# Kernel tuning notes

Hardware: AMD Instinct MI355X
Metric: run time of the kernel (lower is better)

## Reference

```python
import jax, jax.numpy as jnp
import numpy as np

F = 256

def setup_inputs() -> dict:
    key = jax.random.key(0)
    ks = jax.random.split(key, 6)
    s = 1.0 / np.sqrt(F)
    x = jax.random.normal(ks[0], (16, 1024, F), dtype=jnp.float32)
    W_alpha = jax.random.uniform(ks[1], (F, F), minval=-s, maxval=s, dtype=jnp.float32)
    W_beta = jax.random.uniform(ks[2], (F, F), minval=-s, maxval=s, dtype=jnp.float32)
    W_unary = jax.random.uniform(ks[3], (F, F), minval=-s, maxval=s, dtype=jnp.float32)
    b_unary = jax.random.uniform(ks[4], (F,), minval=-s, maxval=s, dtype=jnp.float32)
    W_r = jax.random.uniform(ks[5], (F, F), minval=-s, maxval=s, dtype=jnp.float32)
    return {"x": x, "W_alpha": W_alpha, "W_beta": W_beta, "W_unary": W_unary, "b_unary": b_unary, "W_r": W_r}

def reference(x, W_alpha, W_beta, W_unary, b_unary, W_r):
    # x: [B, N, F]; torch Linear computes x @ W^T (+ b)
    B, N, _ = x.shape
    alpha = jnp.einsum('bnf,gf->bng', x, W_alpha)
    beta = jnp.einsum('bnf,gf->bng', x, W_beta)
    unary = jnp.einsum('bnf,gf->bng', x, W_unary) + b_unary
    # scores: alpha_i . beta_j, diagonal excluded (i == j skipped in loop)
    scores = jnp.einsum('bif,bjf->bij', alpha, beta)
    scores = scores * (1.0 - jnp.eye(N, dtype=x.dtype))
    att = jnp.einsum('bij,bjf->bif', scores, unary) / N
    out = jnp.einsum('bif,gf->big', att, W_r) + x
    return out
```

## Files before the change

kernel.cpp:

```cpp
#include <hip/hip_runtime.h>


typedef __bf16 bf16;
typedef float floatx4 __attribute__((ext_vector_type(4)));
typedef bf16 bf16x8 __attribute__((ext_vector_type(8)));
typedef bf16 bf16x4 __attribute__((ext_vector_type(4)));

constexpr int FD = 256;
constexpr int NB = 16;
constexpr int NN = 1024;
constexpr int RR = NB * NN;

__global__ __launch_bounds__(256)
void prep(const float* __restrict__ Wa, const float* __restrict__ Wb,
          const float* __restrict__ Wu, const float* __restrict__ bu, const float* __restrict__ Wr,
          bf16* __restrict__ Wab, bf16* __restrict__ Wbb, bf16* __restrict__ Wcb,
          float* __restrict__ bc)
{
    const int blk = blockIdx.x, tid = threadIdx.x;
    if (blk < 16) {
        int w = blk >> 3, wb = blk & 7;
        const float* src = (w == 0) ? Wa : Wb;
        bf16* dst = (w == 0) ? Wab : Wbb;
        for (int it = 0; it < 8; it++) {
            int i = wb * 8192 + it * 1024 + tid * 4;
            float4 v = *(const float4*)&src[i];
            bf16x4 o = { (bf16)v.x, (bf16)v.y, (bf16)v.z, (bf16)v.w };
            *(bf16x4*)&dst[i] = o;
        }
    } else if (blk < 80) {
        int j0 = (blk - 16) * 4;
        float acc[4] = {};
        for (int g = 0; g < FD; g++) {
            float wu = Wu[g * FD + tid];
            #pragma unroll
            for (int jr = 0; jr < 4; jr++)
                acc[jr] += Wr[(j0 + jr) * FD + g] * wu;
        }
        #pragma unroll
        for (int jr = 0; jr < 4; jr++)
            Wcb[(j0 + jr) * FD + tid] = (bf16)acc[jr];
    } else {
        float s = 0.0f;
        for (int g = 0; g < FD; g++) s += Wr[tid * FD + g] * bu[g];
        bc[tid] = s;
    }
}

__global__ __launch_bounds__(256)
void proj3(const float* __restrict__ x,
           const bf16* __restrict__ W0, const bf16* __restrict__ W1, const bf16* __restrict__ W2,
           bf16* __restrict__ alpha, bf16* __restrict__ U2,
           bf16* __restrict__ betaT, bf16* __restrict__ U2T,
           const float* __restrict__ bc, float* __restrict__ dpart)
{
    constexpr int BM = 128, BN = 64, BK = 32, LDK = 40;
    __shared__ bf16 As[BM][LDK];
    __shared__ bf16 Bs[3][BN][LDK];
    __shared__ bf16 Tr[64][136];
    const int tid = threadIdx.x;
    const int wave = tid >> 6, lane = tid & 63;
    const int q = lane >> 4, l16 = lane & 15;
    const int bm = blockIdx.y * BM, bn = blockIdx.x * BN;
    const bf16* Wp[3] = { W0, W1, W2 };

    floatx4 acc[3][2][4] = {};

    for (int k0 = 0; k0 < FD; k0 += BK) {
        #pragma unroll
        for (int it = 0; it < 2; it++) {
            int c = tid + it * 256;
            int row = c >> 2, k8 = (c & 3) * 8;
            const float* src = &x[(size_t)(bm + row) * FD + k0 + k8];
            float4 v0 = *(const float4*)src;
            float4 v1 = *(const float4*)(src + 4);
            bf16x8 o = { (bf16)v0.x, (bf16)v0.y, (bf16)v0.z, (bf16)v0.w,
                         (bf16)v1.x, (bf16)v1.y, (bf16)v1.z, (bf16)v1.w };
            *(bf16x8*)&As[row][k8] = o;
        }
        #pragma unroll
        for (int w = 0; w < 3; w++) {
            int row = tid >> 2, k8 = (tid & 3) * 8;
            *(int4*)&Bs[w][row][k8] = *(const int4*)&Wp[w][(size_t)(bn + row) * FD + k0 + k8];
        }
        __syncthreads();
        bf16x8 af[2];
        #pragma unroll
        for (int mi = 0; mi < 2; mi++)
            af[mi] = *(const bf16x8*)&As[wave * 32 + mi * 16 + l16][q * 8];
        #pragma unroll
        for (int w = 0; w < 3; w++) {
            bf16x8 bq[4];
            #pragma unroll
            for (int nj = 0; nj < 4; nj++)
                bq[nj] = *(const bf16x8*)&Bs[w][nj * 16 + l16][q * 8];
            #pragma unroll
            for (int mi = 0; mi < 2; mi++)
                #pragma unroll
                for (int nj = 0; nj < 4; nj++)
                    acc[w][mi][nj] = __builtin_amdgcn_mfma_f32_16x16x32_bf16(af[mi], bq[nj], acc[w][mi][nj], 0, 0, 0);
        }
        __syncthreads();
    }

    const int b = bm >> 10, n0 = bm & (NN - 1);

    #pragma unroll
    for (int mi = 0; mi < 2; mi++)
        #pragma unroll
        for (int i = 0; i < 4; i++) {
            int m = bm + wave * 32 + mi * 16 + q * 4 + i;
            #pragma unroll
            for (int nj = 0; nj < 4; nj++) {
                int n = bn + nj * 16 + l16;
                alpha[(size_t)m * FD + n] = (bf16)acc[0][mi][nj][i];
                U2[(size_t)m * FD + n]    = (bf16)(acc[2][mi][nj][i] + bc[n]);
            }
        }

    #pragma unroll
    for (int mi = 0; mi < 2; mi++)
        #pragma unroll
        for (int i = 0; i < 4; i++) {
            float p = 0.0f;
            #pragma unroll
            for (int nj = 0; nj < 4; nj++)
                p += acc[0][mi][nj][i] * acc[1][mi][nj][i];
            #pragma unroll
            for (int off = 1; off < 16; off <<= 1) p += __shfl_xor(p, off);
            if (l16 == 0) {
                int m = bm + wave * 32 + mi * 16 + q * 4 + i;
                dpart[(size_t)blockIdx.x * RR + m] = p;
            }
        }

    #pragma unroll
    for (int w = 1; w < 3; w++) {
        __syncthreads();
        #pragma unroll
        for (int mi = 0; mi < 2; mi++)
            #pragma unroll
            for (int i = 0; i < 4; i++)
                #pragma unroll
                for (int nj = 0; nj < 4; nj++) {
                    float v = acc[w][mi][nj][i];
                    if (w == 2) v += bc[bn + nj * 16 + l16];
                    Tr[nj * 16 + l16][wave * 32 + mi * 16 + q * 4 + i] = (bf16)v;
                }
        __syncthreads();
        bf16* dst = ((w == 1) ? betaT : U2T) + (size_t)b * FD * NN;
        int row = tid >> 2;
        #pragma unroll
        for (int it = 0; it < 4; it++) {
            int chunk = (tid & 3) * 4 + it;
            bf16x8 v = *(const bf16x8*)&Tr[row][chunk * 8];
            *(bf16x8*)&dst[(size_t)(bn + row) * NN + n0 + chunk * 8] = v;
        }
    }
}

__global__ __launch_bounds__(256)
void m2_mfma(const bf16* __restrict__ U2T, const bf16* __restrict__ betaT, bf16* __restrict__ M2t)
{
    constexpr int LDK = 40;
    __shared__ bf16 As[64][LDK];
    __shared__ bf16 Bs[64][LDK];
    const int tid = threadIdx.x;
    const int wave = tid >> 6, lane = tid & 63;
    const int q = lane >> 4, l16 = lane & 15;
    const int wj = wave >> 1, wk = wave & 1;
    const int b = blockIdx.z;
    const int bj = blockIdx.y * 64, bk = blockIdx.x * 64;
    const bf16* A = U2T + (size_t)b * FD * NN;
    const bf16* B = betaT + (size_t)b * FD * NN;

    floatx4 acc[2][2] = {};
    for (int n0 = 0; n0 < NN; n0 += 32) {
        int row = tid >> 2, k8 = (tid & 3) * 8;
        *(int4*)&As[row][k8] = *(const int4*)&A[(size_t)(bj + row) * NN + n0 + k8];
        *(int4*)&Bs[row][k8] = *(const int4*)&B[(size_t)(bk + row) * NN + n0 + k8];
        __syncthreads();
        bf16x8 af[2], bq[2];
        #pragma unroll
        for (int mi = 0; mi < 2; mi++)
            af[mi] = *(const bf16x8*)&As[wj * 32 + mi * 16 + l16][q * 8];
        #pragma unroll
        for (int kj = 0; kj < 2; kj++)
            bq[kj] = *(const bf16x8*)&Bs[wk * 32 + kj * 16 + l16][q * 8];
        #pragma unroll
        for (int mi = 0; mi < 2; mi++)
            #pragma unroll
            for (int kj = 0; kj < 2; kj++)
                acc[mi][kj] = __builtin_amdgcn_mfma_f32_16x16x32_bf16(af[mi], bq[kj], acc[mi][kj], 0, 0, 0);
        __syncthreads();
    }
    bf16* Mb = M2t + (size_t)b * FD * FD;
    #pragma unroll
    for (int mi = 0; mi < 2; mi++)
        #pragma unroll
        for (int i = 0; i < 4; i++) {
            int j = bj + wj * 32 + mi * 16 + q * 4 + i;
            #pragma unroll
            for (int kj = 0; kj < 2; kj++)
                Mb[(size_t)j * FD + bk + wk * 32 + kj * 16 + l16] = (bf16)acc[mi][kj][i];
        }
}

__global__ __launch_bounds__(256)
void final_mfma(const bf16* __restrict__ alpha, const bf16* __restrict__ M2t,
                const float* __restrict__ dpart, const bf16* __restrict__ U2,
                const float* __restrict__ x, float* __restrict__ out)
{
    constexpr int BM = 128, BN = 64, BK = 32, LDK = 40;
    __shared__ bf16 As[BM][LDK];
    __shared__ bf16 Bs[BN][LDK];
    const int tid = threadIdx.x;
    const int wave = tid >> 6, lane = tid & 63;
    const int q = lane >> 4, l16 = lane & 15;
    const int bm = blockIdx.y * BM, bn = blockIdx.x * BN;
    const bf16* Qb = M2t + (size_t)(bm >> 10) * FD * FD;

    floatx4 acc[2][4] = {};
    for (int k0 = 0; k0 < FD; k0 += BK) {
        int c = tid, row = c >> 2, k8 = (c & 3) * 8;
        *(int4*)&As[row][k8] = *(const int4*)&alpha[(size_t)(bm + row) * FD + k0 + k8];
        c = tid + 256; row = c >> 2; k8 = (c & 3) * 8;
        *(int4*)&As[row][k8] = *(const int4*)&alpha[(size_t)(bm + row) * FD + k0 + k8];
        int rb = tid >> 2, kb8 = (tid & 3) * 8;
        *(int4*)&Bs[rb][kb8] = *(const int4*)&Qb[(size_t)(bn + rb) * FD + k0 + kb8];
        __syncthreads();
        bf16x8 af[2], bq[4];
        #pragma unroll
        for (int mi = 0; mi < 2; mi++)
            af[mi] = *(const bf16x8*)&As[wave * 32 + mi * 16 + l16][q * 8];
        #pragma unroll
        for (int nj = 0; nj < 4; nj++)
            bq[nj] = *(const bf16x8*)&Bs[nj * 16 + l16][q * 8];
        #pragma unroll
        for (int mi = 0; mi < 2; mi++)
            #pragma unroll
            for (int nj = 0; nj < 4; nj++)
                acc[mi][nj] = __builtin_amdgcn_mfma_f32_16x16x32_bf16(af[mi], bq[nj], acc[mi][nj], 0, 0, 0);
        __syncthreads();
    }

    #pragma unroll
    for (int mi = 0; mi < 2; mi++)
        #pragma unroll
        for (int i = 0; i < 4; i++) {
            int m = bm + wave * 32 + mi * 16 + q * 4 + i;
            float d = dpart[m] + dpart[RR + m] + dpart[2 * RR + m] + dpart[3 * RR + m];
            #pragma unroll
            for (int nj = 0; nj < 4; nj++) {
                int n = bn + nj * 16 + l16;
                float v = (acc[mi][nj][i] - d * (float)U2[(size_t)m * FD + n]) * (1.0f / 1024.0f);
                out[(size_t)m * FD + n] = v + x[(size_t)m * FD + n];
            }
        }
}

extern "C" void kernel_launch(void* const* d_in, const int* in_sizes, int n_in,
                              void* d_out, int out_size, void* d_ws, size_t ws_size,
                              hipStream_t stream)
{
    const float* x  = (const float*)d_in[0];
    const float* Wa = (const float*)d_in[1];
    const float* Wb = (const float*)d_in[2];
    const float* Wu = (const float*)d_in[3];
    const float* bu = (const float*)d_in[4];
    const float* Wr = (const float*)d_in[5];
    float* out = (float*)d_out;

    char* w = (char*)d_ws;
    bf16* Wab   = (bf16*)w;  w += (size_t)FD * FD * 2;
    bf16* Wbb   = (bf16*)w;  w += (size_t)FD * FD * 2;
    bf16* Wcb   = (bf16*)w;  w += (size_t)FD * FD * 2;
    float* bc   = (float*)w; w += (size_t)FD * 4;
    bf16* alpha = (bf16*)w;  w += (size_t)RR * FD * 2;
    bf16* U2    = (bf16*)w;  w += (size_t)RR * FD * 2;
    bf16* betaT = (bf16*)w;  w += (size_t)RR * FD * 2;
    bf16* U2T   = (bf16*)w;  w += (size_t)RR * FD * 2;
    bf16* M2t   = (bf16*)w;  w += (size_t)NB * FD * FD * 2;
    float* dpart= (float*)w; w += (size_t)4 * RR * 4;

    dim3 blk(256);

    prep<<<dim3(81), blk, 0, stream>>>(Wa, Wb, Wu, bu, Wr, Wab, Wbb, Wcb, bc);

    proj3<<<dim3(FD / 64, RR / 128), blk, 0, stream>>>(x, Wab, Wbb, Wcb,
                                                       alpha, U2, betaT, U2T, bc, dpart);

    m2_mfma<<<dim3(FD / 64, FD / 64, NB), blk, 0, stream>>>(U2T, betaT, M2t);

    final_mfma<<<dim3(FD / 64, RR / 128), blk, 0, stream>>>(alpha, M2t, dpart, U2, x, out);
}
```

Baseline: 141.1 us.

## Prefetch tiles into registers, coalesce epilogue stores, fold weight conversion into projection

Across the three GEMM kernels, the next K-slice is now loaded into registers while the current tile is computed, overlapping global latency with MFMA work. The row-major alpha/U2 outputs and the M2t output are staged through shared memory so each thread writes 16-byte vectors instead of scattered 2-byte stores. The transposed writes now use packed bf16x4 shared stores. Wa and Wb are converted to bf16 inside proj3 rather than in prep, and prep is rebalanced to one output row per block. Shared padding changes from 40 to 36, which may alter bank conflicts and leaves 16-byte LDS accesses only 8-byte aligned on odd rows.

```diff
diff --git a/kernel.cpp b/kernel.cpp
--- a/kernel.cpp
+++ b/kernel.cpp
@@ -11,35 +11,26 @@
 constexpr int NN = 1024;
 constexpr int RR = NB * NN;
 
+__device__ __forceinline__ bf16x8 cvt8(float4 a, float4 b) {
+    bf16x8 o = { (bf16)a.x, (bf16)a.y, (bf16)a.z, (bf16)a.w,
+                 (bf16)b.x, (bf16)b.y, (bf16)b.z, (bf16)b.w };
+    return o;
+}
+
 __global__ __launch_bounds__(256)
-void prep(const float* __restrict__ Wa, const float* __restrict__ Wb,
-          const float* __restrict__ Wu, const float* __restrict__ bu, const float* __restrict__ Wr,
-          bf16* __restrict__ Wab, bf16* __restrict__ Wbb, bf16* __restrict__ Wcb,
-          float* __restrict__ bc)
+void prep(const float* __restrict__ Wu, const float* __restrict__ bu, const float* __restrict__ Wr,
+          bf16* __restrict__ Wcb, float* __restrict__ bc)
 {
     const int blk = blockIdx.x, tid = threadIdx.x;
-    if (blk < 16) {
-        int w = blk >> 3, wb = blk & 7;
-        const float* src = (w == 0) ? Wa : Wb;
-        bf16* dst = (w == 0) ? Wab : Wbb;
-        for (int it = 0; it < 8; it++) {
-            int i = wb * 8192 + it * 1024 + tid * 4;
-            float4 v = *(const float4*)&src[i];
-            bf16x4 o = { (bf16)v.x, (bf16)v.y, (bf16)v.z, (bf16)v.w };
-            *(bf16x4*)&dst[i] = o;
-        }
-    } else if (blk < 80) {
-        int j0 = (blk - 16) * 4;
-        float acc[4] = {};
-        for (int g = 0; g < FD; g++) {
-            float wu = Wu[g * FD + tid];
-            #pragma unroll
-            for (int jr = 0; jr < 4; jr++)
-                acc[jr] += Wr[(j0 + jr) * FD + g] * wu;
-        }
-        #pragma unroll
-        for (int jr = 0; jr < 4; jr++)
-            Wcb[(j0 + jr) * FD + tid] = (bf16)acc[jr];
+    if (blk < 256) {
+        const int j = blk;
+        float acc = 0.0f;
+        for (int g = 0; g < FD; g += 4) {
+            float4 wr = *(const float4*)&Wr[j * FD + g];
+            acc += wr.x * Wu[g * FD + tid] + wr.y * Wu[(g + 1) * FD + tid]
+                 + wr.z * Wu[(g + 2) * FD + tid] + wr.w * Wu[(g + 3) * FD + tid];
+        }
+        Wcb[j * FD + tid] = (bf16)acc;
     } else {
         float s = 0.0f;
         for (int g = 0; g < FD; g++) s += Wr[tid * FD + g] * bu[g];
@@ -49,41 +40,48 @@
 
 __global__ __launch_bounds__(256)
 void proj3(const float* __restrict__ x,
-           const bf16* __restrict__ W0, const bf16* __restrict__ W1, const bf16* __restrict__ W2,
+           const float* __restrict__ Wa, const float* __restrict__ Wb, const bf16* __restrict__ Wc,
            bf16* __restrict__ alpha, bf16* __restrict__ U2,
            bf16* __restrict__ betaT, bf16* __restrict__ U2T,
            const float* __restrict__ bc, float* __restrict__ dpart)
 {
-    constexpr int BM = 128, BN = 64, BK = 32, LDK = 40;
+    constexpr int BM = 128, BN = 64, BK = 32, LDK = 36;
     __shared__ bf16 As[BM][LDK];
     __shared__ bf16 Bs[3][BN][LDK];
-    __shared__ bf16 Tr[64][136];
+    __shared__ bf16 Tr[8960];
     const int tid = threadIdx.x;
     const int wave = tid >> 6, lane = tid & 63;
     const int q = lane >> 4, l16 = lane & 15;
     const int bm = blockIdx.y * BM, bn = blockIdx.x * BN;
-    const bf16* Wp[3] = { W0, W1, W2 };
+
+    const int rowA0 = tid >> 2,          k8A0 = (tid & 3) * 8;
+    const int rowA1 = (tid + 256) >> 2,  k8A1 = (tid & 3) * 8;
+    const int rowW  = tid >> 2,          k8W  = (tid & 3) * 8;
+
+    bf16x8 pxa0, pxa1, pwa, pwb; int4 pwc;
+#define PROJ_LOAD(KK) do { \
+        const float* s0 = &x[(size_t)(bm + rowA0) * FD + (KK) + k8A0]; \
+        pxa0 = cvt8(*(const float4*)s0, *(const float4*)(s0 + 4)); \
+        const float* s1 = &x[(size_t)(bm + rowA1) * FD + (KK) + k8A1]; \
+        pxa1 = cvt8(*(const float4*)s1, *(const float4*)(s1 + 4)); \
+        const float* sa = &Wa[(size_t)(bn + rowW) * FD + (KK) + k8W]; \
+        pwa = cvt8(*(const float4*)sa, *(const float4*)(sa + 4)); \
+        const float* sb = &Wb[(size_t)(bn + rowW) * FD + (KK) + k8W]; \
+        pwb = cvt8(*(const float4*)sb, *(const float4*)(sb + 4)); \
+        pwc = *(const int4*)&Wc[(size_t)(bn + rowW) * FD + (KK) + k8W]; \
+    } while (0)
 
     floatx4 acc[3][2][4] = {};
+    PROJ_LOAD(0);
 
     for (int k0 = 0; k0 < FD; k0 += BK) {
-        #pragma unroll
-        for (int it = 0; it < 2; it++) {
-            int c = tid + it * 256;
-            int row = c >> 2, k8 = (c & 3) * 8;
-            const float* src = &x[(size_t)(bm + row) * FD + k0 + k8];
-            float4 v0 = *(const float4*)src;
-            float4 v1 = *(const float4*)(src + 4);
-            bf16x8 o = { (bf16)v0.x, (bf16)v0.y, (bf16)v0.z, (bf16)v0.w,
-                         (bf16)v1.x, (bf16)v1.y, (bf16)v1.z, (bf16)v1.w };
-            *(bf16x8*)&As[row][k8] = o;
-        }
-        #pragma unroll
-        for (int w = 0; w < 3; w++) {
-            int row = tid >> 2, k8 = (tid & 3) * 8;
-            *(int4*)&Bs[w][row][k8] = *(const int4*)&Wp[w][(size_t)(bn + row) * FD + k0 + k8];
-        }
-        __syncthreads();
+        *(bf16x8*)&As[rowA0][k8A0] = pxa0;
+        *(bf16x8*)&As[rowA1][k8A1] = pxa1;
+        *(bf16x8*)&Bs[0][rowW][k8W] = pwa;
+        *(bf16x8*)&Bs[1][rowW][k8W] = pwb;
+        *(int4*)&Bs[2][rowW][k8W] = pwc;
+        __syncthreads();
+        if (k0 + BK < FD) PROJ_LOAD(k0 + BK);
         bf16x8 af[2];
         #pragma unroll
         for (int mi = 0; mi < 2; mi++)
@@ -102,21 +100,12 @@
         }
         __syncthreads();
     }
+#undef PROJ_LOAD
 
     const int b = bm >> 10, n0 = bm & (NN - 1);
-
-    #pragma unroll
-    for (int mi = 0; mi < 2; mi++)
-        #pragma unroll
-        for (int i = 0; i < 4; i++) {
-            int m = bm + wave * 32 + mi * 16 + q * 4 + i;
-            #pragma unroll
-            for (int nj = 0; nj < 4; nj++) {
-                int n = bn + nj * 16 + l16;
-                alpha[(size_t)m * FD + n] = (bf16)acc[0][mi][nj][i];
-                U2[(size_t)m * FD + n]    = (bf16)(acc[2][mi][nj][i] + bc[n]);
-            }
-        }
+    float bcv[4];
+    #pragma unroll
+    for (int nj = 0; nj < 4; nj++) bcv[nj] = bc[bn + nj * 16 + l16];
 
     #pragma unroll
     for (int mi = 0; mi < 2; mi++)
@@ -135,25 +124,56 @@
         }
 
     #pragma unroll
-    for (int w = 1; w < 3; w++) {
-        __syncthreads();
-        #pragma unroll
-        for (int mi = 0; mi < 2; mi++)
-            #pragma unroll
-            for (int i = 0; i < 4; i++)
+    for (int pass = 0; pass < 2; pass++) {
+        const int w = pass ? 2 : 0;
+        __syncthreads();
+        #pragma unroll
+        for (int mi = 0; mi < 2; mi++)
+            #pragma unroll
+            for (int i = 0; i < 4; i++) {
+                int ml = wave * 32 + mi * 16 + q * 4 + i;
                 #pragma unroll
                 for (int nj = 0; nj < 4; nj++) {
                     float v = acc[w][mi][nj][i];
-                    if (w == 2) v += bc[bn + nj * 16 + l16];
-                    Tr[nj * 16 + l16][wave * 32 + mi * 16 + q * 4 + i] = (bf16)v;
+                    if (w == 2) v += bcv[nj];
+                    Tr[ml * 68 + nj * 16 + l16] = (bf16)v;
                 }
-        __syncthreads();
-        bf16* dst = ((w == 1) ? betaT : U2T) + (size_t)b * FD * NN;
-        int row = tid >> 2;
+            }
+        __syncthreads();
+        bf16* dst = pass ? U2 : alpha;
         #pragma unroll
         for (int it = 0; it < 4; it++) {
-            int chunk = (tid & 3) * 4 + it;
-            bf16x8 v = *(const bf16x8*)&Tr[row][chunk * 8];
+            int c = tid + it * 256;
+            int row = c >> 3, chunk = c & 7;
+            bf16x8 v = *(const bf16x8*)&Tr[row * 68 + chunk * 8];
+            *(bf16x8*)&dst[(size_t)(bm + row) * FD + bn + chunk * 8] = v;
+        }
+    }
+
+    #pragma unroll
+    for (int pass = 0; pass < 2; pass++) {
+        const int w = pass ? 2 : 1;
+        __syncthreads();
+        #pragma unroll
+        for (int mi = 0; mi < 2; mi++)
+            #pragma unroll
+            for (int nj = 0; nj < 4; nj++) {
+                bf16x4 v4;
+                #pragma unroll
+                for (int i = 0; i < 4; i++) {
+                    float v = acc[w][mi][nj][i];
+                    if (w == 2) v += bcv[nj];
+                    v4[i] = (bf16)v;
+                }
+                *(bf16x4*)&Tr[(nj * 16 + l16) * 140 + wave * 32 + mi * 16 + q * 4] = v4;
+            }
+        __syncthreads();
+        bf16* dst = (pass ? U2T : betaT) + (size_t)b * FD * NN;
+        #pragma unroll
+        for (int it = 0; it < 4; it++) {
+            int c = tid + it * 256;
+            int row = c >> 4, chunk = c & 15;
+            bf16x8 v = *(const bf16x8*)&Tr[row * 140 + chunk * 8];
             *(bf16x8*)&dst[(size_t)(bn + row) * NN + n0 + chunk * 8] = v;
         }
     }
@@ -162,24 +182,28 @@
 __global__ __launch_bounds__(256)
 void m2_mfma(const bf16* __restrict__ U2T, const bf16* __restrict__ betaT, bf16* __restrict__ M2t)
 {
-    constexpr int LDK = 40;
+    constexpr int LDK = 36;
     __shared__ bf16 As[64][LDK];
     __shared__ bf16 Bs[64][LDK];
+    __shared__ bf16 Tr[64 * 68];
     const int tid = threadIdx.x;
     const int wave = tid >> 6, lane = tid & 63;
     const int q = lane >> 4, l16 = lane & 15;
     const int wj = wave >> 1, wk = wave & 1;
     const int b = blockIdx.z;
     const int bj = blockIdx.y * 64, bk = blockIdx.x * 64;
-    const bf16* A = U2T + (size_t)b * FD * NN;
-    const bf16* B = betaT + (size_t)b * FD * NN;
-
+    const int row = tid >> 2, k8 = (tid & 3) * 8;
+    const bf16* Arow = U2T + (size_t)b * FD * NN + (size_t)(bj + row) * NN + k8;
+    const bf16* Brow = betaT + (size_t)b * FD * NN + (size_t)(bk + row) * NN + k8;
+
+    int4 ra = *(const int4*)&Arow[0];
+    int4 rb = *(const int4*)&Brow[0];
     floatx4 acc[2][2] = {};
     for (int n0 = 0; n0 < NN; n0 += 32) {
-        int row = tid >> 2, k8 = (tid & 3) * 8;
-        *(int4*)&As[row][k8] = *(const int4*)&A[(size_t)(bj + row) * NN + n0 + k8];
-        *(int4*)&Bs[row][k8] = *(const int4*)&B[(size_t)(bk + row) * NN + n0 + k8];
-        __syncthreads();
+        *(int4*)&As[row][k8] = ra;
+        *(int4*)&Bs[row][k8] = rb;
+        __syncthreads();
+        if (n0 + 32 < NN) { ra = *(const int4*)&Arow[n0 + 32]; rb = *(const int4*)&Brow[n0 + 32]; }
         bf16x8 af[2], bq[2];
         #pragma unroll
         for (int mi = 0; mi < 2; mi++)
@@ -194,16 +218,25 @@
                 acc[mi][kj] = __builtin_amdgcn_mfma_f32_16x16x32_bf16(af[mi], bq[kj], acc[mi][kj], 0, 0, 0);
         __syncthreads();
     }
+    __syncthreads();
+    #pragma unroll
+    for (int mi = 0; mi < 2; mi++)
+        #pragma unroll
+        for (int i = 0; i < 4; i++) {
+            int jl = wj * 32 + mi * 16 + q * 4 + i;
+            #pragma unroll
+            for (int kj = 0; kj < 2; kj++)
+                Tr[jl * 68 + wk * 32 + kj * 16 + l16] = (bf16)acc[mi][kj][i];
+        }
+    __syncthreads();
     bf16* Mb = M2t + (size_t)b * FD * FD;
     #pragma unroll
-    for (int mi = 0; mi < 2; mi++)
-        #pragma unroll
-        for (int i = 0; i < 4; i++) {
-            int j = bj + wj * 32 + mi * 16 + q * 4 + i;
-            #pragma unroll
-            for (int kj = 0; kj < 2; kj++)
-                Mb[(size_t)j * FD + bk + wk * 32 + kj * 16 + l16] = (bf16)acc[mi][kj][i];
-        }
+    for (int it = 0; it < 2; it++) {
+        int c = tid + it * 256;
+        int r = c >> 3, chunk = c & 7;
+        bf16x8 v = *(const bf16x8*)&Tr[r * 68 + chunk * 8];
+        *(bf16x8*)&Mb[(size_t)(bj + r) * FD + bk + chunk * 8] = v;
+    }
 }
 
 __global__ __launch_bounds__(256)
@@ -211,7 +244,7 @@
                 const float* __restrict__ dpart, const bf16* __restrict__ U2,
                 const float* __restrict__ x, float* __restrict__ out)
 {
-    constexpr int BM = 128, BN = 64, BK = 32, LDK = 40;
+    constexpr int BM = 128, BN = 64, BK = 32, LDK = 36;
     __shared__ bf16 As[BM][LDK];
     __shared__ bf16 Bs[BN][LDK];
     const int tid = threadIdx.x;
@@ -220,15 +253,25 @@
     const int bm = blockIdx.y * BM, bn = blockIdx.x * BN;
     const bf16* Qb = M2t + (size_t)(bm >> 10) * FD * FD;
 
+    const int rowA0 = tid >> 2,         k8A0 = (tid & 3) * 8;
+    const int rowA1 = (tid + 256) >> 2, k8A1 = (tid & 3) * 8;
+    const int rowB  = tid >> 2,         k8B  = (tid & 3) * 8;
+
+    int4 ra0 = *(const int4*)&alpha[(size_t)(bm + rowA0) * FD + k8A0];
+    int4 ra1 = *(const int4*)&alpha[(size_t)(bm + rowA1) * FD + k8A1];
+    int4 rb  = *(const int4*)&Qb[(size_t)(bn + rowB) * FD + k8B];
+
     floatx4 acc[2][4] = {};
     for (int k0 = 0; k0 < FD; k0 += BK) {
-        int c = tid, row = c >> 2, k8 = (c & 3) * 8;
-        *(int4*)&As[row][k8] = *(const int4*)&alpha[(size_t)(bm + row) * FD + k0 + k8];
-        c = tid + 256; row = c >> 2; k8 = (c & 3) * 8;
-        *(int4*)&As[row][k8] = *(const int4*)&alpha[(size_t)(bm + row) * FD + k0 + k8];
-        int rb = tid >> 2, kb8 = (tid & 3) * 8;
-        *(int4*)&Bs[rb][kb8] = *(const int4*)&Qb[(size_t)(bn + rb) * FD + k0 + kb8];
-        __syncthreads();
+        *(int4*)&As[rowA0][k8A0] = ra0;
+        *(int4*)&As[rowA1][k8A1] = ra1;
+        *(int4*)&Bs[rowB][k8B] = rb;
+        __syncthreads();
+        if (k0 + BK < FD) {
+            ra0 = *(const int4*)&alpha[(size_t)(bm + rowA0) * FD + k0 + BK + k8A0];
+            ra1 = *(const int4*)&alpha[(size_t)(bm + rowA1) * FD + k0 + BK + k8A1];
+            rb  = *(const int4*)&Qb[(size_t)(bn + rowB) * FD + k0 + BK + k8B];
+        }
         bf16x8 af[2], bq[4];
         #pragma unroll
         for (int mi = 0; mi < 2; mi++)
@@ -272,8 +315,6 @@
     float* out = (float*)d_out;
 
     char* w = (char*)d_ws;
-    bf16* Wab   = (bf16*)w;  w += (size_t)FD * FD * 2;
-    bf16* Wbb   = (bf16*)w;  w += (size_t)FD * FD * 2;
     bf16* Wcb   = (bf16*)w;  w += (size_t)FD * FD * 2;
     float* bc   = (float*)w; w += (size_t)FD * 4;
     bf16* alpha = (bf16*)w;  w += (size_t)RR * FD * 2;
@@ -285,9 +326,9 @@
 
     dim3 blk(256);
 
-    prep<<<dim3(81), blk, 0, stream>>>(Wa, Wb, Wu, bu, Wr, Wab, Wbb, Wcb, bc);
-
-    proj3<<<dim3(FD / 64, RR / 128), blk, 0, stream>>>(x, Wab, Wbb, Wcb,
+    prep<<<dim3(257), blk, 0, stream>>>(Wu, bu, Wr, Wcb, bc);
+
+    proj3<<<dim3(FD / 64, RR / 128), blk, 0, stream>>>(x, Wa, Wb, Wcb,
                                                        alpha, U2, betaT, U2T, bc, dpart);
 
     m2_mfma<<<dim3(FD / 64, FD / 64, NB), blk, 0, stream>>>(U2T, betaT, M2t);
```

New measurement: 127.8 us. -9.4%, faster.
